# Optimization experiments

Hardware: AMD Instinct MI355X
Metric: run time of the kernel (lower is better)

## Reference

```python
import jax, jax.numpy as jnp
import numpy as np

N_NODES = 100000
N_EDGES = 600000
IN_FEATS = 128
HIDDEN = 128


def sage_conv(x, src, dst, w_l, b_l, w_r, num_nodes):
    """PyG SAGEConv with mean aggregation.
    out = mean_{j in N(i)} x_j @ w_l.T + b_l + x_i @ w_r.T
    src/dst: int arrays [E]; messages flow src -> dst.
    """
    msgs = x[src]                                             # [E, F] gather
    summed = jax.ops.segment_sum(msgs, dst, num_segments=num_nodes)  # [N, F]
    ones = jnp.ones((src.shape[0],), dtype=x.dtype)
    deg = jax.ops.segment_sum(ones, dst, num_segments=num_nodes)     # [N]
    agg = summed / jnp.maximum(deg, 1.0)[:, None]             # mean, safe for deg=0
    return agg @ w_l.T + b_l + x @ w_r.T


def setup_inputs() -> dict:
    key = jax.random.key(0)
    ks = jax.random.split(key, 10)

    def glorot(k, shape):
        fan_in = shape[-1]
        bound = 1.0 / np.sqrt(fan_in)
        return jax.random.uniform(k, shape, jnp.float32, -bound, bound)

    x = jax.random.normal(ks[0], (N_NODES, IN_FEATS), dtype=jnp.float32)
    xedge = jax.random.randint(ks[1], (2, N_EDGES), 0, N_NODES, dtype=jnp.int64)
    return {
        "x": x,
        "xedge": xedge,
        # SAGEConv 1 (in_feats -> hidden): lin_l (with bias) + lin_r (no bias)
        "w1_l": glorot(ks[2], (HIDDEN, IN_FEATS)),
        "b1_l": glorot(ks[3], (HIDDEN,)),
        "w1_r": glorot(ks[4], (HIDDEN, IN_FEATS)),
        # SAGEConv 2 (hidden -> hidden)
        "w2_l": glorot(ks[5], (HIDDEN, HIDDEN)),
        "b2_l": glorot(ks[6], (HIDDEN,)),
        "w2_r": glorot(ks[7], (HIDDEN, HIDDEN)),
        # Decoder: Linear(hidden -> hidden)
        "w_dec": glorot(ks[8], (HIDDEN, HIDDEN)),
        "b_dec": glorot(ks[9], (HIDDEN,)),
    }


def reference(x, xedge, w1_l, b1_l, w1_r, w2_l, b2_l, w2_r, w_dec, b_dec):
    src, dst = xedge[0], xedge[1]
    n = x.shape[0]
    h = sage_conv(x, src, dst, w1_l, b1_l, w1_r, n)   # conv1
    h = jax.nn.relu(h)
    # dropout omitted (deterministic eval semantics)
    h = sage_conv(h, src, dst, w2_l, b2_l, w2_r, n)   # conv2 -> encoder output
    dx = h @ w_dec.T + b_dec                          # decoder
    return (h, dx)
```

## Files before the change

kernel.cpp:

```cpp
#include <hip/hip_runtime.h>

typedef __attribute__((ext_vector_type(8))) short bf16x8;
typedef __attribute__((ext_vector_type(4))) float f32x4;
typedef unsigned int uint;
typedef unsigned short ushort;

#define NFEAT 128

__device__ __forceinline__ ushort f2b(float f) {
    uint u = __float_as_uint(f);
    u = (u + 0x7fffu + ((u >> 16) & 1u)) >> 16;
    return (ushort)u;
}

__device__ __forceinline__ void gload_lds16(const ushort* g, char* lds) {
    __builtin_amdgcn_global_load_lds((const __attribute__((address_space(1))) void*)g,
                                     (__attribute__((address_space(3))) void*)lds, 16, 0, 0);
}

__global__ __launch_bounds__(256) void prep(
    const float* __restrict__ x, ushort* __restrict__ x_bf, long nx,
    const float* __restrict__ w1l, const float* __restrict__ w1r,
    const float* __restrict__ w2l, const float* __restrict__ w2r,
    const float* __restrict__ wd,
    ushort* __restrict__ wc1, ushort* __restrict__ wc2, ushort* __restrict__ wdec,
    const int* __restrict__ dst, int* __restrict__ deg, int E, int nCvt)
{
    const int b = blockIdx.x;
    if (b < nCvt) {
        long i = ((long)b * 256 + threadIdx.x) * 4;
        if (i < nx) {
            float4 v = *(const float4*)(x + i);
            ushort4 o;
            o.x = f2b(v.x); o.y = f2b(v.y); o.z = f2b(v.z); o.w = f2b(v.w);
            *(ushort4*)(x_bf + i) = o;
        }
    } else if (b < nCvt + 256) {
        const int bb = b - nCvt;
        const int i = (bb & 127) * 256 + threadIdx.x;
        const int row = i >> 8, col = i & 255;
        const float* wl = (bb < 128) ? w1l : w2l;
        const float* wr = (bb < 128) ? w1r : w2r;
        ushort* dstw = (bb < 128) ? wc1 : wc2;
        float v = (col < 128) ? wl[row * 128 + col] : wr[row * 128 + col - 128];
        dstw[i] = f2b(v);
    } else if (b < nCvt + 320) {
        const int i = (b - nCvt - 256) * 256 + threadIdx.x;
        wdec[i] = f2b(wd[i]);
    } else {
        const int e = (b - nCvt - 320) * 256 + threadIdx.x;
        if (e < E) atomicAdd(&deg[dst[e]], 1);
    }
}

__global__ __launch_bounds__(256) void scan_blocks(const int* __restrict__ in, int* __restrict__ out,
                                                   int* __restrict__ bsum, int n) {
    __shared__ int lds[256];
    const int t = threadIdx.x;
    const int base = blockIdx.x * 1024 + t * 4;
    int a[4];
#pragma unroll
    for (int q = 0; q < 4; ++q) a[q] = (base + q < n) ? in[base + q] : 0;
    const int tsum = a[0] + a[1] + a[2] + a[3];
    lds[t] = tsum;
    __syncthreads();
    for (int off = 1; off < 256; off <<= 1) {
        int v = (t >= off) ? lds[t - off] : 0;
        __syncthreads();
        lds[t] += v;
        __syncthreads();
    }
    const int excl = lds[t] - tsum;
    if (t == 255) bsum[blockIdx.x] = lds[255];
    int r = excl;
#pragma unroll
    for (int q = 0; q < 4; ++q) {
        if (base + q < n) out[base + q] = r;
        r += a[q];
    }
}

__global__ __launch_bounds__(256) void scan_add(int* __restrict__ row_off, int* __restrict__ pos,
                                                const int* __restrict__ bsum, int n, int E) {
    const int i = blockIdx.x * 256 + threadIdx.x;
    const int cb = blockIdx.x >> 2;
    const int lane = threadIdx.x & 63;
    int v = 0;
    if (lane < cb) v += bsum[lane];
    if (lane + 64 < cb) v += bsum[lane + 64];
#pragma unroll
    for (int off = 1; off < 64; off <<= 1) v += __shfl_xor(v, off);
    if (i < n) {
        const int r = row_off[i] + v;
        row_off[i] = r;
        pos[i] = r;
    }
    if (i == 0) row_off[n] = E;
}

__global__ void fill_csr(const int* __restrict__ src, const int* __restrict__ dst,
                         int* __restrict__ pos, int* __restrict__ perm, int E) {
    const int e = blockIdx.x * blockDim.x + threadIdx.x;
    if (e < E) {
        const int p = atomicAdd(&pos[dst[e]], 1);
        perm[p] = src[e];
    }
}

__global__ __launch_bounds__(256) void gather_mean_bf(const int* __restrict__ row_off,
                                                      const int* __restrict__ perm,
                                                      const ushort* __restrict__ feat,
                                                      ushort* __restrict__ out, int n) {
    const int node = (blockIdx.x * 256 + threadIdx.x) >> 4;
    if (node >= n) return;
    const int chunk = threadIdx.x & 15;
    const int lo = row_off[node], hi = row_off[node + 1];
    float acc[8] = {0.f, 0.f, 0.f, 0.f, 0.f, 0.f, 0.f, 0.f};
    int i = lo;
    for (; i + 3 < hi; i += 4) {
        const int s0 = perm[i], s1 = perm[i + 1], s2 = perm[i + 2], s3 = perm[i + 3];
        const uint4 v0 = *(const uint4*)(feat + (size_t)s0 * NFEAT + chunk * 8);
        const uint4 v1 = *(const uint4*)(feat + (size_t)s1 * NFEAT + chunk * 8);
        const uint4 v2 = *(const uint4*)(feat + (size_t)s2 * NFEAT + chunk * 8);
        const uint4 v3 = *(const uint4*)(feat + (size_t)s3 * NFEAT + chunk * 8);
        const uint p0[4] = {v0.x, v0.y, v0.z, v0.w};
        const uint p1[4] = {v1.x, v1.y, v1.z, v1.w};
        const uint p2[4] = {v2.x, v2.y, v2.z, v2.w};
        const uint p3[4] = {v3.x, v3.y, v3.z, v3.w};
#pragma unroll
        for (int q = 0; q < 4; ++q) {
            acc[2 * q]     += __uint_as_float(p0[q] << 16) + __uint_as_float(p1[q] << 16)
                            + __uint_as_float(p2[q] << 16) + __uint_as_float(p3[q] << 16);
            acc[2 * q + 1] += __uint_as_float(p0[q] & 0xffff0000u) + __uint_as_float(p1[q] & 0xffff0000u)
                            + __uint_as_float(p2[q] & 0xffff0000u) + __uint_as_float(p3[q] & 0xffff0000u);
        }
    }
    for (; i < hi; ++i) {
        const int s = perm[i];
        const uint4 v = *(const uint4*)(feat + (size_t)s * NFEAT + chunk * 8);
        const uint p[4] = {v.x, v.y, v.z, v.w};
#pragma unroll
        for (int q = 0; q < 4; ++q) {
            acc[2 * q]     += __uint_as_float(p[q] << 16);
            acc[2 * q + 1] += __uint_as_float(p[q] & 0xffff0000u);
        }
    }
    const float inv = 1.0f / fmaxf((float)(hi - lo), 1.0f);
    ushort o[8] __attribute__((aligned(16)));
#pragma unroll
    for (int q = 0; q < 8; ++q) o[q] = f2b(acc[q] * inv);
    *(uint4*)(out + (size_t)node * NFEAT + chunk * 8) = *(const uint4*)o;
}

template <bool RELU, bool DEC>
__global__ __launch_bounds__(256) void sage_mfma(
    const ushort* __restrict__ Amean, const ushort* __restrict__ Axin,
    const ushort* __restrict__ Wcat, const float* __restrict__ bias,
    const ushort* __restrict__ Wdec, const float* __restrict__ bdec,
    float* __restrict__ outf, ushort* __restrict__ outb,
    float* __restrict__ dxp, int n)
{
    __shared__ uint4 smem4[2048];
    char* As = (char*)smem4;
    char* Ws = As + 16384;
    const int t = threadIdx.x;
    const int m0 = blockIdx.x * 128;
    const int lane = t & 63;
    const int wid = t >> 6;
    const int lrow = lane & 15;
    const int lq = lane >> 4;

    f32x4 acc[2][8];
#pragma unroll
    for (int m = 0; m < 2; ++m)
#pragma unroll
        for (int nn = 0; nn < 8; ++nn) acc[m][nn] = (f32x4){0.f, 0.f, 0.f, 0.f};

    for (int kt = 0; kt < 4; ++kt) {
        const ushort* Abase = (kt < 2) ? Amean : Axin;
        const int co = (kt & 1) * 64;
#pragma unroll
        for (int i = 0; i < 4; ++i) {
            const int row = i * 32 + wid * 8 + (lane >> 3);
            const int c = (lane & 7) ^ (row & 7);
            int gm = m0 + row;
            if (gm >= n) gm = n - 1;
            gload_lds16(Abase + (size_t)gm * NFEAT + co + c * 8,
                        As + i * 4096 + wid * 1024);
            gload_lds16(Wcat + (size_t)row * 256 + kt * 64 + c * 8,
                        Ws + i * 4096 + wid * 1024);
        }
        __syncthreads();
#pragma unroll
        for (int ks = 0; ks < 2; ++ks) {
            bf16x8 af[2], bfr[8];
#pragma unroll
            for (int m = 0; m < 2; ++m) {
                const int row = wid * 32 + m * 16 + lrow;
                af[m] = *(const bf16x8*)(As + row * 128 + (((ks * 4 + lq) * 16) ^ ((row & 7) << 4)));
            }
#pragma unroll
            for (int nn = 0; nn < 8; ++nn) {
                const int row = nn * 16 + lrow;
                bfr[nn] = *(const bf16x8*)(Ws + row * 128 + (((ks * 4 + lq) * 16) ^ ((row & 7) << 4)));
            }
#pragma unroll
            for (int m = 0; m < 2; ++m)
#pragma unroll
                for (int nn = 0; nn < 8; ++nn)
                    acc[m][nn] = __builtin_amdgcn_mfma_f32_16x16x32_bf16(bfr[nn], af[m], acc[m][nn], 0, 0, 0);
        }
        __syncthreads();
    }
    char* Lh = As;
#pragma unroll
    for (int m = 0; m < 2; ++m) {
        const int row = wid * 32 + m * 16 + lrow;
        const int grow = m0 + row;
#pragma unroll
        for (int nn = 0; nn < 8; ++nn) {
            const int colb = nn * 16 + lq * 4;
            const float4 bv = *(const float4*)(bias + colb);
            float v0 = acc[m][nn][0] + bv.x;
            float v1 = acc[m][nn][1] + bv.y;
            float v2 = acc[m][nn][2] + bv.z;
            float v3 = acc[m][nn][3] + bv.w;
            if (RELU) {
                v0 = fmaxf(v0, 0.f); v1 = fmaxf(v1, 0.f);
                v2 = fmaxf(v2, 0.f); v3 = fmaxf(v3, 0.f);
            }
            ushort4 ob;
            ob.x = f2b(v0); ob.y = f2b(v1); ob.z = f2b(v2); ob.w = f2b(v3);
            if (grow < n) {
                if (outf) *(float4*)(outf + (size_t)grow * NFEAT + colb) = make_float4(v0, v1, v2, v3);
                if (outb) *(ushort4*)(outb + (size_t)grow * NFEAT + colb) = ob;
            }
            if (DEC)
                *(ushort4*)(Lh + row * 256 + ((colb * 2) ^ ((row & 7) << 4))) = ob;
        }
    }
    if (DEC) {
        f32x4 acc2[2][8];
#pragma unroll
        for (int m = 0; m < 2; ++m)
#pragma unroll
            for (int nn = 0; nn < 8; ++nn) acc2[m][nn] = (f32x4){0.f, 0.f, 0.f, 0.f};
#pragma unroll
        for (int ks = 0; ks < 4; ++ks) {
            bf16x8 af2[2], bf2[8];
#pragma unroll
            for (int m = 0; m < 2; ++m) {
                const int row = wid * 32 + m * 16 + lrow;
                af2[m] = *(const bf16x8*)(Lh + row * 256 + ((ks * 64 + lq * 16) ^ ((row & 7) << 4)));
            }
#pragma unroll
            for (int nn = 0; nn < 8; ++nn)
                bf2[nn] = *(const bf16x8*)(Wdec + (size_t)(nn * 16 + lrow) * NFEAT + ks * 32 + lq * 8);
#pragma unroll
            for (int m = 0; m < 2; ++m)
#pragma unroll
                for (int nn = 0; nn < 8; ++nn)
                    acc2[m][nn] = __builtin_amdgcn_mfma_f32_16x16x32_bf16(bf2[nn], af2[m], acc2[m][nn], 0, 0, 0);
        }
#pragma unroll
        for (int m = 0; m < 2; ++m) {
            const int grow = m0 + wid * 32 + m * 16 + lrow;
            if (grow < n) {
#pragma unroll
                for (int nn = 0; nn < 8; ++nn) {
                    const int colb = nn * 16 + lq * 4;
                    const float4 bv = *(const float4*)(bdec + colb);
                    *(float4*)(dxp + (size_t)grow * NFEAT + colb) =
                        make_float4(acc2[m][nn][0] + bv.x, acc2[m][nn][1] + bv.y,
                                    acc2[m][nn][2] + bv.z, acc2[m][nn][3] + bv.w);
                }
            }
        }
    }
}

extern "C" void kernel_launch(void* const* d_in, const int* in_sizes, int n_in,
                              void* d_out, int out_size, void* d_ws, size_t ws_size,
                              hipStream_t stream) {
    const float* x     = (const float*)d_in[0];
    const int*   xedge = (const int*)d_in[1];
    const float* w1_l  = (const float*)d_in[2];
    const float* b1_l  = (const float*)d_in[3];
    const float* w1_r  = (const float*)d_in[4];
    const float* w2_l  = (const float*)d_in[5];
    const float* b2_l  = (const float*)d_in[6];
    const float* w2_r  = (const float*)d_in[7];
    const float* w_dec = (const float*)d_in[8];
    const float* b_dec = (const float*)d_in[9];

    const int N = in_sizes[0] / NFEAT;
    const int E = in_sizes[1] / 2;
    const int* src = xedge;
    const int* dst = xedge + E;

    float* h_out = (float*)d_out;
    float* dxp   = h_out + (size_t)N * NFEAT;

    char* ws = (char*)d_ws;
    ushort* x_bf    = (ushort*)ws;
    ushort* h1_bf   = x_bf   + (size_t)N * NFEAT;
    ushort* mean_bf = h1_bf  + (size_t)N * NFEAT;
    ushort* wc1     = mean_bf + (size_t)N * NFEAT;
    ushort* wc2     = wc1 + 128 * 256;
    ushort* wdec    = wc2 + 128 * 256;
    int* deg        = (int*)(wdec + 128 * 128);
    int* row_off    = deg + N;
    int* pos        = row_off + (N + 1);
    int* bsum       = pos + N;
    int* perm       = bsum + 256;

    hipMemsetAsync(deg, 0, (size_t)N * sizeof(int), stream);
    const long nx = (long)N * NFEAT;
    const int nCvt = (int)((nx / 4 + 255) / 256);
    const int histB = (E + 255) / 256;
    prep<<<nCvt + 320 + histB, 256, 0, stream>>>(x, x_bf, nx, w1_l, w1_r, w2_l, w2_r, w_dec,
                                                 wc1, wc2, wdec, dst, deg, E, nCvt);

    const int nb = (N + 1023) / 1024;
    scan_blocks<<<nb, 256, 0, stream>>>(deg, row_off, bsum, N);
    scan_add<<<(N + 255) / 256, 256, 0, stream>>>(row_off, pos, bsum, N, E);
    fill_csr<<<histB, 256, 0, stream>>>(src, dst, pos, perm, E);

    const int gb = (N + 127) / 128;
    const int ggb = (N * 16 + 255) / 256;

    gather_mean_bf<<<ggb, 256, 0, stream>>>(row_off, perm, x_bf, mean_bf, N);
    sage_mfma<true, false><<<gb, 256, 0, stream>>>(mean_bf, x_bf, wc1, b1_l,
                                                   nullptr, nullptr, nullptr, h1_bf, nullptr, N);

    gather_mean_bf<<<ggb, 256, 0, stream>>>(row_off, perm, h1_bf, mean_bf, N);
    sage_mfma<false, true><<<gb, 256, 0, stream>>>(mean_bf, h1_bf, wc2, b2_l,
                                                   wdec, b_dec, h_out, nullptr, dxp, N);

    (void)n_in; (void)out_size; (void)ws_size;
}
```

Baseline: 199.8 us.

## Prepack weights in MFMA fragment order and double-buffer A tiles per wave

```diff
diff --git a/kernel.cpp b/kernel.cpp
--- a/kernel.cpp
+++ b/kernel.cpp
@@ -37,16 +37,23 @@
         }
     } else if (b < nCvt + 256) {
         const int bb = b - nCvt;
-        const int i = (bb & 127) * 256 + threadIdx.x;
-        const int row = i >> 8, col = i & 255;
+        const int j = (bb & 127) * 256 + threadIdx.x;
+        const int e = j & 7, lq = (j >> 3) & 3, lr = (j >> 5) & 15, nn = (j >> 9) & 7;
+        const int ks = (j >> 12) & 1, kt = (j >> 13) & 3;
+        const int col = nn * 16 + lr;
+        const int k = kt * 64 + ks * 32 + lq * 8 + e;
         const float* wl = (bb < 128) ? w1l : w2l;
         const float* wr = (bb < 128) ? w1r : w2r;
         ushort* dstw = (bb < 128) ? wc1 : wc2;
-        float v = (col < 128) ? wl[row * 128 + col] : wr[row * 128 + col - 128];
-        dstw[i] = f2b(v);
+        float v = (k < 128) ? wl[col * 128 + k] : wr[col * 128 + (k - 128)];
+        dstw[j] = f2b(v);
     } else if (b < nCvt + 320) {
-        const int i = (b - nCvt - 256) * 256 + threadIdx.x;
-        wdec[i] = f2b(wd[i]);
+        const int j = (b - nCvt - 256) * 256 + threadIdx.x;
+        const int e = j & 7, lq = (j >> 3) & 3, lr = (j >> 5) & 15, nn = (j >> 9) & 7;
+        const int ks = (j >> 12) & 3;
+        const int col = nn * 16 + lr;
+        const int k = ks * 32 + lq * 8 + e;
+        wdec[j] = f2b(wd[col * 128 + k]);
     } else {
         const int e = (b - nCvt - 320) * 256 + threadIdx.x;
         if (e < E) atomicAdd(&deg[dst[e]], 1);
@@ -116,13 +123,20 @@
     const int chunk = threadIdx.x & 15;
     const int lo = row_off[node], hi = row_off[node + 1];
     float acc[8] = {0.f, 0.f, 0.f, 0.f, 0.f, 0.f, 0.f, 0.f};
-    int i = lo;
-    for (; i + 3 < hi; i += 4) {
-        const int s0 = perm[i], s1 = perm[i + 1], s2 = perm[i + 2], s3 = perm[i + 3];
-        const uint4 v0 = *(const uint4*)(feat + (size_t)s0 * NFEAT + chunk * 8);
-        const uint4 v1 = *(const uint4*)(feat + (size_t)s1 * NFEAT + chunk * 8);
-        const uint4 v2 = *(const uint4*)(feat + (size_t)s2 * NFEAT + chunk * 8);
-        const uint4 v3 = *(const uint4*)(feat + (size_t)s3 * NFEAT + chunk * 8);
+    const uint4 z = make_uint4(0, 0, 0, 0);
+    for (int i = lo; i < hi; i += 4) {
+        const int rem = hi - i;
+        const int s0 = perm[i];
+        const int s1 = perm[(rem > 1) ? i + 1 : i];
+        const int s2 = perm[(rem > 2) ? i + 2 : i];
+        const int s3 = perm[(rem > 3) ? i + 3 : i];
+        uint4 v0 = *(const uint4*)(feat + (size_t)s0 * NFEAT + chunk * 8);
+        uint4 v1 = *(const uint4*)(feat + (size_t)s1 * NFEAT + chunk * 8);
+        uint4 v2 = *(const uint4*)(feat + (size_t)s2 * NFEAT + chunk * 8);
+        uint4 v3 = *(const uint4*)(feat + (size_t)s3 * NFEAT + chunk * 8);
+        if (rem < 2) v1 = z;
+        if (rem < 3) v2 = z;
+        if (rem < 4) v3 = z;
         const uint p0[4] = {v0.x, v0.y, v0.z, v0.w};
         const uint p1[4] = {v1.x, v1.y, v1.z, v1.w};
         const uint p2[4] = {v2.x, v2.y, v2.z, v2.w};
@@ -135,16 +149,6 @@
                             + __uint_as_float(p2[q] & 0xffff0000u) + __uint_as_float(p3[q] & 0xffff0000u);
         }
     }
-    for (; i < hi; ++i) {
-        const int s = perm[i];
-        const uint4 v = *(const uint4*)(feat + (size_t)s * NFEAT + chunk * 8);
-        const uint p[4] = {v.x, v.y, v.z, v.w};
-#pragma unroll
-        for (int q = 0; q < 4; ++q) {
-            acc[2 * q]     += __uint_as_float(p[q] << 16);
-            acc[2 * q + 1] += __uint_as_float(p[q] & 0xffff0000u);
-        }
-    }
     const float inv = 1.0f / fmaxf((float)(hi - lo), 1.0f);
     ushort o[8] __attribute__((aligned(16)));
 #pragma unroll
@@ -155,14 +159,13 @@
 template <bool RELU, bool DEC>
 __global__ __launch_bounds__(256) void sage_mfma(
     const ushort* __restrict__ Amean, const ushort* __restrict__ Axin,
-    const ushort* __restrict__ Wcat, const float* __restrict__ bias,
-    const ushort* __restrict__ Wdec, const float* __restrict__ bdec,
+    const ushort* __restrict__ Wf, const float* __restrict__ bias,
+    const ushort* __restrict__ Wdecf, const float* __restrict__ bdec,
     float* __restrict__ outf, ushort* __restrict__ outb,
     float* __restrict__ dxp, int n)
 {
     __shared__ uint4 smem4[2048];
     char* As = (char*)smem4;
-    char* Ws = As + 16384;
     const int t = threadIdx.x;
     const int m0 = blockIdx.x * 128;
     const int lane = t & 63;
@@ -170,48 +173,57 @@
     const int lrow = lane & 15;
     const int lq = lane >> 4;
 
-    f32x4 acc[2][8];
-#pragma unroll
-    for (int m = 0; m < 2; ++m)
-#pragma unroll
-        for (int nn = 0; nn < 8; ++nn) acc[m][nn] = (f32x4){0.f, 0.f, 0.f, 0.f};
-
-    for (int kt = 0; kt < 4; ++kt) {
+    auto stage = [&](int b, int kt) {
         const ushort* Abase = (kt < 2) ? Amean : Axin;
         const int co = (kt & 1) * 64;
 #pragma unroll
         for (int i = 0; i < 4; ++i) {
-            const int row = i * 32 + wid * 8 + (lane >> 3);
-            const int c = (lane & 7) ^ (row & 7);
+            const int chunk = i * 64 + lane;
+            const int rloc = chunk >> 3, c = chunk & 7;
+            const int row = wid * 32 + rloc;
             int gm = m0 + row;
             if (gm >= n) gm = n - 1;
-            gload_lds16(Abase + (size_t)gm * NFEAT + co + c * 8,
-                        As + i * 4096 + wid * 1024);
-            gload_lds16(Wcat + (size_t)row * 256 + kt * 64 + c * 8,
-                        Ws + i * 4096 + wid * 1024);
-        }
-        __syncthreads();
+            gload_lds16(Abase + (size_t)gm * NFEAT + co + (c ^ (row & 7)) * 8,
+                        As + b * 16384 + wid * 4096 + i * 1024);
+        }
+    };
+
+    f32x4 acc[2][8];
+#pragma unroll
+    for (int m = 0; m < 2; ++m)
+#pragma unroll
+        for (int nn = 0; nn < 8; ++nn) acc[m][nn] = (f32x4){0.f, 0.f, 0.f, 0.f};
+
+    stage(0, 0);
+    stage(1, 1);
+    for (int kt = 0; kt < 4; ++kt) {
+        if (kt < 3) asm volatile("s_waitcnt vmcnt(4)" ::: "memory");
+        else        asm volatile("s_waitcnt vmcnt(0)" ::: "memory");
+        const int b = kt & 1;
 #pragma unroll
         for (int ks = 0; ks < 2; ++ks) {
             bf16x8 af[2], bfr[8];
 #pragma unroll
             for (int m = 0; m < 2; ++m) {
-                const int row = wid * 32 + m * 16 + lrow;
-                af[m] = *(const bf16x8*)(As + row * 128 + (((ks * 4 + lq) * 16) ^ ((row & 7) << 4)));
-            }
-#pragma unroll
-            for (int nn = 0; nn < 8; ++nn) {
-                const int row = nn * 16 + lrow;
-                bfr[nn] = *(const bf16x8*)(Ws + row * 128 + (((ks * 4 + lq) * 16) ^ ((row & 7) << 4)));
-            }
+                const int r = m * 16 + lrow;
+                const int row = wid * 32 + r;
+                af[m] = *(const bf16x8*)(As + b * 16384 + wid * 4096 + r * 128 +
+                                         (((ks * 4 + lq) * 16) ^ ((row & 7) << 4)));
+            }
+#pragma unroll
+            for (int nn = 0; nn < 8; ++nn)
+                bfr[nn] = *(const bf16x8*)(Wf + (size_t)((((kt * 2 + ks) * 8 + nn) * 64) + lrow * 4 + lq) * 8);
 #pragma unroll
             for (int m = 0; m < 2; ++m)
 #pragma unroll
                 for (int nn = 0; nn < 8; ++nn)
                     acc[m][nn] = __builtin_amdgcn_mfma_f32_16x16x32_bf16(bfr[nn], af[m], acc[m][nn], 0, 0, 0);
         }
-        __syncthreads();
-    }
+        if (kt + 2 < 4) stage(b, kt + 2);
+    }
+
+    if (DEC) __syncthreads();
+
     char* Lh = As;
 #pragma unroll
     for (int m = 0; m < 2; ++m) {
@@ -255,7 +267,7 @@
             }
 #pragma unroll
             for (int nn = 0; nn < 8; ++nn)
-                bf2[nn] = *(const bf16x8*)(Wdec + (size_t)(nn * 16 + lrow) * NFEAT + ks * 32 + lq * 8);
+                bf2[nn] = *(const bf16x8*)(Wdecf + (size_t)(((ks * 8 + nn) * 64) + lrow * 4 + lq) * 8);
 #pragma unroll
             for (int m = 0; m < 2; ++m)
 #pragma unroll
```

After: 207.4 us. +3.8%, slower.
